# Performance work log

Hardware: AMD Instinct MI355X
Metric: run time of the kernel (lower is better)

The kernel has to match this reference:

```python
import jax, jax.numpy as jnp
import numpy as np

B, S, D_IN, D_ATT = 8, 2048, 512, 512

def setup_inputs() -> dict:
    key = jax.random.key(0)
    ks = jax.random.split(key, 7)
    sc = 1.0 / np.sqrt(D_IN)
    return {
        "x": jax.random.normal(ks[0], (B, S, D_IN), dtype=jnp.float32),
        "Wq": jax.random.uniform(ks[1], (D_IN, D_ATT), jnp.float32, -sc, sc),
        "bq": jax.random.uniform(ks[2], (D_ATT,), jnp.float32, -sc, sc),
        "Wk": jax.random.uniform(ks[3], (D_IN, D_ATT), jnp.float32, -sc, sc),
        "bk": jax.random.uniform(ks[4], (D_ATT,), jnp.float32, -sc, sc),
        "Wv": jax.random.uniform(ks[5], (D_IN, D_ATT), jnp.float32, -sc, sc),
        "bv": jax.random.uniform(ks[6], (D_ATT,), jnp.float32, -sc, sc),
    }

def reference(x, Wq, bq, Wk, bk, Wv, bv):
    # Linear projections: [B, S, D_att]
    q = jnp.einsum("bsd,de->bse", x, Wq) + bq
    k = jnp.einsum("bsd,de->bse", x, Wk) + bk
    v = jnp.einsum("bsd,de->bse", x, Wv) + bv
    # Full scores matrix [B, S, S]; note: NO 1/sqrt(d) scaling in original.
    scores = jnp.einsum("bqe,bke->bqk", q, k)
    attn = jax.nn.softmax(scores, axis=-1)
    return jnp.einsum("bqk,bke->bqe", attn, v)
```

## Files before the change

kernel.cpp:

```cpp
#include <hip/hip_runtime.h>
#include <cstdint>
#include <cstddef>


#define SEQ 2048
#define DIM 512
#define NB 8
#define BSZ (NB * SEQ)

typedef __attribute__((ext_vector_type(8))) _Float16 half8;
typedef __attribute__((ext_vector_type(4))) float f32x4;

__device__ __forceinline__ unsigned short f2h(float f) {
  _Float16 h = (_Float16)f;
  return __builtin_bit_cast(unsigned short, h);
}
__device__ __forceinline__ half8 ld_frag(const unsigned short* p) {
  return *(const half8*)(const void*)p;
}
__device__ __forceinline__ void gl_lds16(const unsigned short* g, unsigned short* l) {
  __builtin_amdgcn_global_load_lds(
      (__attribute__((address_space(1))) void*)g,
      (__attribute__((address_space(3))) void*)l, 16, 0, 0);
}

__global__ __launch_bounds__(256) void cvt_x_kernel(
    const float* __restrict__ X, unsigned short* __restrict__ xh)
{
  size_t i0 = ((size_t)blockIdx.x * 256 + threadIdx.x) * 8;
  float4 a = *(const float4*)&X[i0];
  float4 b = *(const float4*)&X[i0 + 4];
  ushort4 o0; o0.x = f2h(a.x); o0.y = f2h(a.y); o0.z = f2h(a.z); o0.w = f2h(a.w);
  ushort4 o1; o1.x = f2h(b.x); o1.y = f2h(b.y); o1.z = f2h(b.z); o1.w = f2h(b.w);
  *(ushort4*)&xh[i0] = o0;
  *(ushort4*)&xh[i0 + 4] = o1;
}

__global__ __launch_bounds__(256) void cvt_w_kernel(
    const float* __restrict__ Wq, const float* __restrict__ Wk,
    const float* __restrict__ Wv, unsigned short* __restrict__ Wt)
{
  const int z = blockIdx.z;
  const float* W = (z == 0) ? Wq : (z == 1) ? Wk : Wv;
  unsigned short* out = Wt + (size_t)z * DIM * DIM;
  const int k0 = blockIdx.x * 64, n0 = blockIdx.y * 64;
  const int t = threadIdx.x;
  __shared__ unsigned short tl[64 * 72];
#pragma unroll
  for (int i = 0; i < 4; i++) {
    int f = t + 256 * i;
    int kr = f >> 4, c4 = (f & 15) * 4;
    float4 v = *(const float4*)&W[(size_t)(k0 + kr) * DIM + n0 + c4];
    tl[(c4 + 0) * 72 + kr] = f2h(v.x);
    tl[(c4 + 1) * 72 + kr] = f2h(v.y);
    tl[(c4 + 2) * 72 + kr] = f2h(v.z);
    tl[(c4 + 3) * 72 + kr] = f2h(v.w);
  }
  __syncthreads();
#pragma unroll
  for (int i = 0; i < 2; i++) {
    int f = t + 256 * i;
    int nr = f >> 3, k8 = (f & 7) * 8;
    *(uint4*)&out[(size_t)(n0 + nr) * DIM + k0 + k8] = *(const uint4*)&tl[nr * 72 + k8];
  }
}

__global__ __launch_bounds__(256) void proj_kernel(
    const unsigned short* __restrict__ xh, const unsigned short* __restrict__ Wt,
    const float* __restrict__ bq, const float* __restrict__ bk,
    const float* __restrict__ bv, unsigned short* __restrict__ outbase)
{
  const int z = blockIdx.z;
  const unsigned short* Wz = Wt + (size_t)z * DIM * DIM;
  const float* bias = (z == 0) ? bq : (z == 1) ? bk : bv;
  unsigned short* out = outbase + (size_t)z * BSZ * DIM;
  const int m0 = blockIdx.x * 128, n0 = blockIdx.y * 128;
  const int t = threadIdx.x, lane = t & 63, wave = t >> 6;
  const int wrow = (wave >> 1) * 64, wcol = (wave & 1) * 64;
  const int lr = lane & 15, lq = (lane >> 4) * 8;

  __shared__ unsigned short sm[128 * 132];
  unsigned short* As = sm;
  unsigned short* Bs = sm + 128 * 64;

  f32x4 acc[4][4];
  const f32x4 zero = {0.f, 0.f, 0.f, 0.f};
#pragma unroll
  for (int r = 0; r < 4; r++)
#pragma unroll
    for (int c = 0; c < 4; c++) acc[r][c] = zero;

  for (int k0 = 0; k0 < DIM; k0 += 64) {
    __syncthreads();
#pragma unroll
    for (int i = 0; i < 4; i++) {
      int f = t + 256 * i;
      int row = f >> 3, c8 = (f & 7) * 8;
      gl_lds16(&xh[(size_t)(m0 + row) * DIM + k0 + c8], &As[i * 2048 + wave * 512]);
      gl_lds16(&Wz[(size_t)(n0 + row) * DIM + k0 + c8], &Bs[i * 2048 + wave * 512]);
    }
    __syncthreads();
#pragma unroll
    for (int kk = 0; kk < 64; kk += 32) {
      half8 a[4], b[4];
#pragma unroll
      for (int r = 0; r < 4; r++) a[r] = ld_frag(&As[(wrow + 16 * r + lr) * 64 + kk + lq]);
#pragma unroll
      for (int c = 0; c < 4; c++) b[c] = ld_frag(&Bs[(wcol + 16 * c + lr) * 64 + kk + lq]);
#pragma unroll
      for (int r = 0; r < 4; r++)
#pragma unroll
        for (int c = 0; c < 4; c++)
          acc[r][c] = __builtin_amdgcn_mfma_f32_16x16x32_f16(a[r], b[c], acc[r][c], 0, 0, 0);
    }
  }
  __syncthreads();
#pragma unroll
  for (int c = 0; c < 4; c++) {
    float bb = bias[n0 + wcol + 16 * c + lr];
#pragma unroll
    for (int r = 0; r < 4; r++)
#pragma unroll
      for (int e = 0; e < 4; e++)
        sm[(wrow + 16 * r + (lane >> 4) * 4 + e) * 132 + wcol + 16 * c + lr] =
            f2h(acc[r][c][e] + bb);
  }
  __syncthreads();
#pragma unroll
  for (int i = 0; i < 8; i++) {
    int f = t + 256 * i;
    int row = f >> 4, c8 = (f & 15) * 8;
    *(uint4*)&out[(size_t)(m0 + row) * DIM + n0 + c8] = *(const uint4*)&sm[row * 132 + c8];
  }
}

__global__ __launch_bounds__(256) void vtrans_kernel(
    const unsigned short* __restrict__ vh, unsigned short* __restrict__ vt)
{
  const int b = blockIdx.z;
  const int s0 = blockIdx.x * 64, n0 = blockIdx.y * 64;
  const int t = threadIdx.x;
  __shared__ unsigned short tl[64 * 72];
#pragma unroll
  for (int i = 0; i < 2; i++) {
    int f = t + 256 * i;
    int sr = f >> 3, c8 = (f & 7) * 8;
    uint4 raw = *(const uint4*)&vh[((size_t)b * SEQ + s0 + sr) * DIM + n0 + c8];
    unsigned short u[8];
    *(uint4*)u = raw;
#pragma unroll
    for (int j = 0; j < 8; j++) tl[(c8 + j) * 72 + sr] = u[j];
  }
  __syncthreads();
#pragma unroll
  for (int i = 0; i < 2; i++) {
    int f = t + 256 * i;
    int nr = f >> 3, s8 = (f & 7) * 8;
    *(uint4*)&vt[((size_t)b * DIM + n0 + nr) * SEQ + s0 + s8] = *(const uint4*)&tl[nr * 72 + s8];
  }
}

__global__ __launch_bounds__(256, 1) void flash_kernel(
    const unsigned short* __restrict__ Qb, const unsigned short* __restrict__ Kb,
    const unsigned short* __restrict__ Vtb, float* __restrict__ Ob)
{
  const int zb = blockIdx.x & 7;
  const int q0 = (blockIdx.x >> 3) * 64;
  const unsigned short* Q = Qb + (size_t)zb * SEQ * DIM;
  const unsigned short* K = Kb + (size_t)zb * SEQ * DIM;
  const unsigned short* V = Vtb + (size_t)zb * DIM * SEQ;
  float* Out = Ob + (size_t)zb * SEQ * DIM;

  const int t = threadIdx.x, lane = t & 63, wave = t >> 6;
  const int lr = lane & 15, lq4 = lane >> 4;
  const float L2E = 1.4426950408889634f;

  __shared__ unsigned short Kbuf[128 * 256];
  __shared__ unsigned short Pbuf[64 * 132];
  float* Obuf = (float*)Kbuf;

  half8 qf[16];
#pragma unroll
  for (int dst = 0; dst < 512; dst += 256) {
    __syncthreads();
#pragma unroll
    for (int i = 0; i < 8; i++) {
      int f = t + 256 * i;
      int row = f >> 5, c32 = f & 31;
      int gc = c32 ^ (row & 7);
      gl_lds16(&Q[(size_t)(q0 + row) * DIM + dst + gc * 8], &Kbuf[i * 2048 + wave * 512]);
    }
    __syncthreads();
#pragma unroll
    for (int ks = 0; ks < 8; ks++) {
      int row = 16 * wave + lr;
      int g = ks * 4 + lq4;
      qf[dst / 32 + ks] = ld_frag(&Kbuf[row * 256 + ((g ^ (row & 7)) << 3)]);
    }
  }

  f32x4 acc[32];
  const f32x4 zero = {0.f, 0.f, 0.f, 0.f};
#pragma unroll
  for (int ob = 0; ob < 32; ob++) acc[ob] = zero;
  float m_run[4], l_run[4];
#pragma unroll
  for (int e = 0; e < 4; e++) { m_run[e] = -__builtin_inff(); l_run[e] = 0.f; }

  for (int kt = 0; kt < SEQ / 128; kt++) {
    f32x4 sacc[8];
#pragma unroll
    for (int c = 0; c < 8; c++) sacc[c] = zero;
#pragma unroll
    for (int dst = 0; dst < 512; dst += 256) {
      __syncthreads();
#pragma unroll
      for (int i = 0; i < 16; i++) {
        int f = t + 256 * i;
        int row = f >> 5, c32 = f & 31;
        int gc = c32 ^ (row & 7);
        gl_lds16(&K[(size_t)(kt * 128 + row) * DIM + dst + gc * 8],
                 &Kbuf[i * 2048 + wave * 512]);
      }
      __syncthreads();
#pragma unroll
      for (int ks = 0; ks < 8; ks++) {
        half8 qa = qf[dst / 32 + ks];
#pragma unroll
        for (int c = 0; c < 8; c++) {
          int row = 16 * c + lr;
          int g = ks * 4 + lq4;
          half8 bf = ld_frag(&Kbuf[row * 256 + ((g ^ (row & 7)) << 3)]);
          sacc[c] = __builtin_amdgcn_mfma_f32_16x16x32_f16(qa, bf, sacc[c], 0, 0, 0);
        }
      }
    }

    float mnew[4], alpha[4];
#pragma unroll
    for (int e = 0; e < 4; e++) {
      float mx = sacc[0][e];
#pragma unroll
      for (int c = 1; c < 8; c++) mx = fmaxf(mx, sacc[c][e]);
      mx = fmaxf(mx, __shfl_xor(mx, 1, 64));
      mx = fmaxf(mx, __shfl_xor(mx, 2, 64));
      mx = fmaxf(mx, __shfl_xor(mx, 4, 64));
      mx = fmaxf(mx, __shfl_xor(mx, 8, 64));
      mnew[e] = fmaxf(m_run[e], mx);
      alpha[e] = exp2f((m_run[e] - mnew[e]) * L2E);
      m_run[e] = mnew[e];
    }
#pragma unroll
    for (int e = 0; e < 4; e++) {
      float sum = 0.f;
#pragma unroll
      for (int c = 0; c < 8; c++) {
        float p = exp2f((sacc[c][e] - mnew[e]) * L2E);
        sum += p;
        Pbuf[(wave * 16 + lq4 * 4 + e) * 132 + 16 * c + lr] = f2h(p);
      }
      sum += __shfl_xor(sum, 1, 64);
      sum += __shfl_xor(sum, 2, 64);
      sum += __shfl_xor(sum, 4, 64);
      sum += __shfl_xor(sum, 8, 64);
      l_run[e] = alpha[e] * l_run[e] + sum;
    }
#pragma unroll
    for (int ob = 0; ob < 32; ob++)
#pragma unroll
      for (int e = 0; e < 4; e++) acc[ob][e] *= alpha[e];

    __syncthreads();
    half8 pf[4];
#pragma unroll
    for (int kc = 0; kc < 4; kc++)
      pf[kc] = ld_frag(&Pbuf[(wave * 16 + lr) * 132 + kc * 32 + lq4 * 8]);
#pragma unroll
    for (int dst = 0; dst < 512; dst += 256) {
      __syncthreads();
#pragma unroll
      for (int i = 0; i < 16; i++) {
        int f = t + 256 * i;
        int row = f >> 4, c16 = f & 15;
        int gc = c16 ^ (row & 7);
        gl_lds16(&V[(size_t)(dst + row) * SEQ + kt * 128 + gc * 8],
                 &Kbuf[i * 2048 + wave * 512]);
      }
      __syncthreads();
#pragma unroll
      for (int kc = 0; kc < 4; kc++)
#pragma unroll
        for (int c = 0; c < 16; c++) {
          int row = 16 * c + lr;
          int g = kc * 4 + lq4;
          half8 vf = ld_frag(&Kbuf[row * 128 + ((g ^ (row & 7)) << 3)]);
          acc[dst / 16 + c] =
              __builtin_amdgcn_mfma_f32_16x16x32_f16(pf[kc], vf, acc[dst / 16 + c], 0, 0, 0);
        }
    }
  }

  float inv[4];
#pragma unroll
  for (int e = 0; e < 4; e++) inv[e] = 1.0f / l_run[e];
#pragma unroll
  for (int dst = 0; dst < 512; dst += 64) {
    __syncthreads();
#pragma unroll
    for (int c = 0; c < 4; c++)
#pragma unroll
      for (int e = 0; e < 4; e++)
        Obuf[(wave * 16 + lq4 * 4 + e) * 68 + 16 * c + lr] = acc[dst / 16 + c][e] * inv[e];
    __syncthreads();
#pragma unroll
    for (int i = 0; i < 4; i++) {
      int f = t + 256 * i;
      int row = f >> 4, c4 = (f & 15) * 4;
      *(float4*)&Out[(size_t)(q0 + row) * DIM + dst + c4] = *(const float4*)&Obuf[row * 68 + c4];
    }
  }
}

extern "C" void kernel_launch(void* const* d_in, const int* in_sizes, int n_in,
                              void* d_out, int out_size, void* d_ws, size_t ws_size,
                              hipStream_t stream)
{
  const float* X  = (const float*)d_in[0];
  const float* Wq = (const float*)d_in[1];
  const float* bq = (const float*)d_in[2];
  const float* Wk = (const float*)d_in[3];
  const float* bk = (const float*)d_in[4];
  const float* Wv = (const float*)d_in[5];
  const float* bv = (const float*)d_in[6];
  float* Out = (float*)d_out;

  char* ws = (char*)d_ws;
  const size_t MB = 1u << 20;
  unsigned short* qh = (unsigned short*)(ws);
  unsigned short* kh = (unsigned short*)(ws + 16 * MB);
  unsigned short* vh = (unsigned short*)(ws + 32 * MB);
  unsigned short* vt = (unsigned short*)(ws + 48 * MB);
  unsigned short* xh = (unsigned short*)(ws + 48 * MB);
  unsigned short* Wt = (unsigned short*)(ws + 64 * MB);

  cvt_x_kernel<<<dim3(BSZ * DIM / 2048), 256, 0, stream>>>(X, xh);
  cvt_w_kernel<<<dim3(8, 8, 3), 256, 0, stream>>>(Wq, Wk, Wv, Wt);
  proj_kernel<<<dim3(BSZ / 128, DIM / 128, 3), 256, 0, stream>>>(
      xh, Wt, bq, bk, bv, qh);
  vtrans_kernel<<<dim3(SEQ / 64, DIM / 64, NB), 256, 0, stream>>>(vh, vt);
  flash_kernel<<<dim3(NB * SEQ / 64), 256, 0, stream>>>(qh, kh, vt, Out);
}
```

Measured before the change: 319.6 us.

## Split KV sequence across two wave groups per block and merge softmax states

Each flash block now runs 512 threads as two independent 256-thread groups. Each group walks half of the key/value tiles with its own LDS staging buffers, and the partial (max, sum, accumulator) states are merged through shared memory at the end. Q fragments are loaded straight from global memory instead of going through LDS. The MFMA operands are transposed so each lane keeps a single row statistic, which simplifies the max and sum reductions. K/V tiles are staged in 128-column chunks with a wider XOR swizzle. The aim is to double the waves per block, giving more latency hiding and more parallel work. The cost is more block-wide barriers shared by both groups, larger LDS use, and an extra merge pass.

```diff
diff --git a/kernel.cpp b/kernel.cpp
--- a/kernel.cpp
+++ b/kernel.cpp
@@ -160,7 +160,7 @@
   }
 }
 
-__global__ __launch_bounds__(256, 1) void flash_kernel(
+__global__ __launch_bounds__(512, 2) void flash_kernel(
     const unsigned short* __restrict__ Qb, const unsigned short* __restrict__ Kb,
     const unsigned short* __restrict__ Vtb, float* __restrict__ Ob)
 {
@@ -171,152 +171,173 @@
   const unsigned short* V = Vtb + (size_t)zb * DIM * SEQ;
   float* Out = Ob + (size_t)zb * SEQ * DIM;
 
-  const int t = threadIdx.x, lane = t & 63, wave = t >> 6;
+  const int t = threadIdx.x;
+  const int lane = t & 63;
+  const int wg = (t >> 6) & 3;
+  const int g = t >> 8;
+  const int tg = t & 255;
   const int lr = lane & 15, lq4 = lane >> 4;
   const float L2E = 1.4426950408889634f;
 
-  __shared__ unsigned short Kbuf[128 * 256];
-  __shared__ unsigned short Pbuf[64 * 132];
-  float* Obuf = (float*)Kbuf;
-
+  __shared__ unsigned short sm[50176];
+  __shared__ float ml[2][64][2];
+  unsigned short* KV = sm + g * 16384;
+  unsigned short* Pb = sm + 32768 + g * 8704;
+  float* Obuf = (float*)sm;
+
+  const unsigned short* qp = &Q[(size_t)(q0 + 16 * wg + lr) * DIM + lq4 * 8];
   half8 qf[16];
 #pragma unroll
-  for (int dst = 0; dst < 512; dst += 256) {
-    __syncthreads();
-#pragma unroll
-    for (int i = 0; i < 8; i++) {
-      int f = t + 256 * i;
-      int row = f >> 5, c32 = f & 31;
-      int gc = c32 ^ (row & 7);
-      gl_lds16(&Q[(size_t)(q0 + row) * DIM + dst + gc * 8], &Kbuf[i * 2048 + wave * 512]);
-    }
-    __syncthreads();
-#pragma unroll
-    for (int ks = 0; ks < 8; ks++) {
-      int row = 16 * wave + lr;
-      int g = ks * 4 + lq4;
-      qf[dst / 32 + ks] = ld_frag(&Kbuf[row * 256 + ((g ^ (row & 7)) << 3)]);
-    }
-  }
+  for (int ks = 0; ks < 16; ks++) qf[ks] = ld_frag(&qp[ks * 32]);
 
   f32x4 acc[32];
   const f32x4 zero = {0.f, 0.f, 0.f, 0.f};
 #pragma unroll
   for (int ob = 0; ob < 32; ob++) acc[ob] = zero;
-  float m_run[4], l_run[4];
-#pragma unroll
-  for (int e = 0; e < 4; e++) { m_run[e] = -__builtin_inff(); l_run[e] = 0.f; }
-
-  for (int kt = 0; kt < SEQ / 128; kt++) {
+  float m_run = -__builtin_inff(), l_run = 0.f;
+
+  for (int j = 0; j < 8; j++) {
+    const int ktg = g * 8 + j;
+
     f32x4 sacc[8];
 #pragma unroll
     for (int c = 0; c < 8; c++) sacc[c] = zero;
 #pragma unroll
-    for (int dst = 0; dst < 512; dst += 256) {
+    for (int dch = 0; dch < 4; dch++) {
+      const int dst = dch * 128;
       __syncthreads();
 #pragma unroll
-      for (int i = 0; i < 16; i++) {
-        int f = t + 256 * i;
-        int row = f >> 5, c32 = f & 31;
-        int gc = c32 ^ (row & 7);
-        gl_lds16(&K[(size_t)(kt * 128 + row) * DIM + dst + gc * 8],
-                 &Kbuf[i * 2048 + wave * 512]);
+      for (int i = 0; i < 8; i++) {
+        int f = tg + 256 * i;
+        int row = f >> 4, c16 = f & 15;
+        int sc = c16 ^ (row & 15);
+        gl_lds16(&K[(size_t)(ktg * 128 + row) * DIM + dst + sc * 8],
+                 &KV[i * 2048 + wg * 512]);
       }
       __syncthreads();
 #pragma unroll
-      for (int ks = 0; ks < 8; ks++) {
-        half8 qa = qf[dst / 32 + ks];
+      for (int ks2 = 0; ks2 < 4; ks2++) {
+        half8 qb = qf[dch * 4 + ks2];
 #pragma unroll
         for (int c = 0; c < 8; c++) {
           int row = 16 * c + lr;
-          int g = ks * 4 + lq4;
-          half8 bf = ld_frag(&Kbuf[row * 256 + ((g ^ (row & 7)) << 3)]);
-          sacc[c] = __builtin_amdgcn_mfma_f32_16x16x32_f16(qa, bf, sacc[c], 0, 0, 0);
+          int p = ((ks2 << 2) + lq4) ^ lr;
+          half8 kf = ld_frag(&KV[row * 128 + p * 8]);
+          sacc[c] = __builtin_amdgcn_mfma_f32_16x16x32_f16(kf, qb, sacc[c], 0, 0, 0);
         }
       }
     }
 
-    float mnew[4], alpha[4];
-#pragma unroll
-    for (int e = 0; e < 4; e++) {
-      float mx = sacc[0][e];
-#pragma unroll
-      for (int c = 1; c < 8; c++) mx = fmaxf(mx, sacc[c][e]);
-      mx = fmaxf(mx, __shfl_xor(mx, 1, 64));
-      mx = fmaxf(mx, __shfl_xor(mx, 2, 64));
-      mx = fmaxf(mx, __shfl_xor(mx, 4, 64));
-      mx = fmaxf(mx, __shfl_xor(mx, 8, 64));
-      mnew[e] = fmaxf(m_run[e], mx);
-      alpha[e] = exp2f((m_run[e] - mnew[e]) * L2E);
-      m_run[e] = mnew[e];
-    }
-#pragma unroll
-    for (int e = 0; e < 4; e++) {
-      float sum = 0.f;
+    float mx = sacc[0][0];
+#pragma unroll
+    for (int c = 0; c < 8; c++)
+#pragma unroll
+      for (int e = 0; e < 4; e++) mx = fmaxf(mx, sacc[c][e]);
+    mx = fmaxf(mx, __shfl_xor(mx, 16, 64));
+    mx = fmaxf(mx, __shfl_xor(mx, 32, 64));
+    float mnew = fmaxf(m_run, mx);
+    float alpha = exp2f((m_run - mnew) * L2E);
+    m_run = mnew;
+
+    float sum = 0.f;
+#pragma unroll
+    for (int c = 0; c < 8; c++) {
+      float p0 = exp2f((sacc[c][0] - mnew) * L2E);
+      float p1 = exp2f((sacc[c][1] - mnew) * L2E);
+      float p2 = exp2f((sacc[c][2] - mnew) * L2E);
+      float p3 = exp2f((sacc[c][3] - mnew) * L2E);
+      sum += (p0 + p1) + (p2 + p3);
+      ushort4 pk;
+      pk.x = f2h(p0); pk.y = f2h(p1); pk.z = f2h(p2); pk.w = f2h(p3);
+      *(ushort4*)&Pb[(16 * wg + lr) * 136 + 16 * c + lq4 * 4] = pk;
+    }
+    sum += __shfl_xor(sum, 16, 64);
+    sum += __shfl_xor(sum, 32, 64);
+    l_run = alpha * l_run + sum;
+
+#pragma unroll
+    for (int ob = 0; ob < 32; ob++) {
+      acc[ob][0] *= alpha; acc[ob][1] *= alpha;
+      acc[ob][2] *= alpha; acc[ob][3] *= alpha;
+    }
+
+    half8 pf[4];
+#pragma unroll
+    for (int kc = 0; kc < 4; kc++)
+      pf[kc] = ld_frag(&Pb[(16 * wg + lr) * 136 + kc * 32 + lq4 * 8]);
+#pragma unroll
+    for (int dch = 0; dch < 4; dch++) {
+      const int dst = dch * 128;
+      __syncthreads();
+#pragma unroll
+      for (int i = 0; i < 8; i++) {
+        int f = tg + 256 * i;
+        int row = f >> 4, c16 = f & 15;
+        int sc = c16 ^ (row & 15);
+        gl_lds16(&V[(size_t)(dst + row) * SEQ + ktg * 128 + sc * 8],
+                 &KV[i * 2048 + wg * 512]);
+      }
+      __syncthreads();
 #pragma unroll
       for (int c = 0; c < 8; c++) {
-        float p = exp2f((sacc[c][e] - mnew[e]) * L2E);
-        sum += p;
-        Pbuf[(wave * 16 + lq4 * 4 + e) * 132 + 16 * c + lr] = f2h(p);
-      }
-      sum += __shfl_xor(sum, 1, 64);
-      sum += __shfl_xor(sum, 2, 64);
-      sum += __shfl_xor(sum, 4, 64);
-      sum += __shfl_xor(sum, 8, 64);
-      l_run[e] = alpha[e] * l_run[e] + sum;
-    }
-#pragma unroll
-    for (int ob = 0; ob < 32; ob++)
-#pragma unroll
-      for (int e = 0; e < 4; e++) acc[ob][e] *= alpha[e];
-
-    __syncthreads();
-    half8 pf[4];
-#pragma unroll
-    for (int kc = 0; kc < 4; kc++)
-      pf[kc] = ld_frag(&Pbuf[(wave * 16 + lr) * 132 + kc * 32 + lq4 * 8]);
-#pragma unroll
-    for (int dst = 0; dst < 512; dst += 256) {
-      __syncthreads();
-#pragma unroll
-      for (int i = 0; i < 16; i++) {
-        int f = t + 256 * i;
-        int row = f >> 4, c16 = f & 15;
-        int gc = c16 ^ (row & 7);
-        gl_lds16(&V[(size_t)(dst + row) * SEQ + kt * 128 + gc * 8],
-                 &Kbuf[i * 2048 + wave * 512]);
-      }
-      __syncthreads();
-#pragma unroll
-      for (int kc = 0; kc < 4; kc++)
-#pragma unroll
-        for (int c = 0; c < 16; c++) {
-          int row = 16 * c + lr;
-          int g = kc * 4 + lq4;
-          half8 vf = ld_frag(&Kbuf[row * 128 + ((g ^ (row & 7)) << 3)]);
-          acc[dst / 16 + c] =
-              __builtin_amdgcn_mfma_f32_16x16x32_f16(pf[kc], vf, acc[dst / 16 + c], 0, 0, 0);
+        int row = 16 * c + lr;
+#pragma unroll
+        for (int kc = 0; kc < 4; kc++) {
+          int p = ((kc << 2) + lq4) ^ lr;
+          half8 vf = ld_frag(&KV[row * 128 + p * 8]);
+          acc[dch * 8 + c] =
+              __builtin_amdgcn_mfma_f32_16x16x32_f16(vf, pf[kc], acc[dch * 8 + c], 0, 0, 0);
         }
-    }
-  }
-
-  float inv[4];
-#pragma unroll
-  for (int e = 0; e < 4; e++) inv[e] = 1.0f / l_run[e];
-#pragma unroll
-  for (int dst = 0; dst < 512; dst += 64) {
-    __syncthreads();
-#pragma unroll
-    for (int c = 0; c < 4; c++)
-#pragma unroll
-      for (int e = 0; e < 4; e++)
-        Obuf[(wave * 16 + lq4 * 4 + e) * 68 + 16 * c + lr] = acc[dst / 16 + c][e] * inv[e];
+      }
+    }
+  }
+
+  if (lq4 == 0) {
+    ml[g][16 * wg + lr][0] = m_run;
+    ml[g][16 * wg + lr][1] = l_run;
+  }
+  __syncthreads();
+  const int qrow = 16 * wg + lr;
+  float m0 = ml[0][qrow][0], l0 = ml[0][qrow][1];
+  float m1 = ml[1][qrow][0], l1 = ml[1][qrow][1];
+  float mM = fmaxf(m0, m1);
+  float a0 = exp2f((m0 - mM) * L2E), a1 = exp2f((m1 - mM) * L2E);
+  float inv = 1.0f / (a0 * l0 + a1 * l1);
+  float myscale = (g == 0) ? a0 : a1;
+
+#pragma unroll
+  for (int dch = 0; dch < 4; dch++) {
+    __syncthreads();
+    if (g == 1) {
+#pragma unroll
+      for (int c = 0; c < 8; c++) {
+        f32x4 v = acc[dch * 8 + c];
+        float4 w; w.x = v[0] * myscale; w.y = v[1] * myscale;
+        w.z = v[2] * myscale; w.w = v[3] * myscale;
+        *(float4*)&Obuf[qrow * 132 + 16 * c + lq4 * 4] = w;
+      }
+    }
+    __syncthreads();
+    if (g == 0) {
+#pragma unroll
+      for (int c = 0; c < 8; c++) {
+        f32x4 v = acc[dch * 8 + c];
+        float4 r = *(const float4*)&Obuf[qrow * 132 + 16 * c + lq4 * 4];
+        float4 w;
+        w.x = (v[0] * myscale + r.x) * inv;
+        w.y = (v[1] * myscale + r.y) * inv;
+        w.z = (v[2] * myscale + r.z) * inv;
+        w.w = (v[3] * myscale + r.w) * inv;
+        *(float4*)&Obuf[qrow * 132 + 16 * c + lq4 * 4] = w;
+      }
+    }
     __syncthreads();
 #pragma unroll
     for (int i = 0; i < 4; i++) {
-      int f = t + 256 * i;
-      int row = f >> 4, c4 = (f & 15) * 4;
-      *(float4*)&Out[(size_t)(q0 + row) * DIM + dst + c4] = *(const float4*)&Obuf[row * 68 + c4];
+      int idx = t + 512 * i;
+      int row = idx >> 5, c4 = (idx & 31) * 4;
+      *(float4*)&Out[(size_t)(q0 + row) * DIM + dch * 128 + c4] =
+          *(const float4*)&Obuf[row * 132 + c4];
     }
   }
 }
@@ -348,5 +369,5 @@
   proj_kernel<<<dim3(BSZ / 128, DIM / 128, 3), 256, 0, stream>>>(
       xh, Wt, bq, bk, bv, qh);
   vtrans_kernel<<<dim3(SEQ / 64, DIM / 64, NB), 256, 0, stream>>>(vh, vt);
-  flash_kernel<<<dim3(NB * SEQ / 64), 256, 0, stream>>>(qh, kh, vt, Out);
-}
+  flash_kernel<<<dim3(NB * SEQ / 64), 512, 0, stream>>>(qh, kh, vt, Out);
+}
```

Measured after the change: 413.2 us. 1.29x slower.
